# Optimization experiments

Measured on AMD Instinct MI355X. Metric: run time of the kernel, lower is better.

Reference implementation:

```python
import jax, jax.numpy as jnp
import numpy as np

NUM_HEADS = 16
TOP_K = 2
ROPE_BASE = 10000.0
LN_EPS = 1e-5


def _rope_sin_cos(S, D, dtype):
    # D = head_dim; inv_freq over even indices, shape [D//2]
    inv_freq = 1.0 / (ROPE_BASE ** (jnp.arange(0, D, 2, dtype=jnp.float32) / D))
    freqs = jnp.arange(S, dtype=jnp.float32)[:, None] * inv_freq[None, :]  # [S, D//2]
    sin = jnp.sin(freqs).astype(dtype)[None, :, None, :]  # [1,S,1,D//2]
    cos = jnp.cos(freqs).astype(dtype)[None, :, None, :]
    return sin, cos


def _apply_rope(x, sin, cos):
    # x: [B,S,H,D]; rotate interleaved even/odd pairs
    x1, x2 = x[..., 0::2], x[..., 1::2]
    r1 = x1 * cos - x2 * sin
    r2 = x1 * sin + x2 * cos
    return jnp.stack([r1, r2], axis=-1).reshape(x.shape)


def _layer_norm(x, w, b):
    mu = jnp.mean(x, axis=-1, keepdims=True)
    var = jnp.mean(jnp.square(x - mu), axis=-1, keepdims=True)
    return (x - mu) * jax.lax.rsqrt(var + LN_EPS) * w + b


def reference(x, in_proj_w, in_proj_b, out_proj_w, out_proj_b,
              gate_w, gate_b, expert_w, expert_b,
              ln1_w, ln1_b, ln2_w, ln2_b):
    B, S, E = x.shape
    H = NUM_HEADS
    D = E // H

    # --- RoPE on q and k (per-head) ---
    xh = x.reshape(B, S, H, D)
    sin, cos = _rope_sin_cos(S, D, x.dtype)
    q_in = _apply_rope(xh, sin, cos).reshape(B, S, E)
    k_in = q_in  # q = k in the module
    v_in = x

    # --- MultiheadAttention (eval, causal mask) ---
    Wq, Wk, Wv = jnp.split(in_proj_w, 3, axis=0)  # each [E,E]
    bq, bk, bv = jnp.split(in_proj_b, 3, axis=0)
    q = (q_in @ Wq.T + bq).reshape(B, S, H, D)
    k = (k_in @ Wk.T + bk).reshape(B, S, H, D)
    v = (v_in @ Wv.T + bv).reshape(B, S, H, D)

    scale = 1.0 / jnp.sqrt(jnp.asarray(D, dtype=x.dtype))
    scores = jnp.einsum('bqhd,bkhd->bhqk', q, k) * scale  # [B,H,S,S]
    causal = jnp.tril(jnp.ones((S, S), dtype=bool))
    scores = jnp.where(causal[None, None], scores, jnp.asarray(-jnp.inf, dtype=scores.dtype))
    attn = jax.nn.softmax(scores, axis=-1)
    ctx = jnp.einsum('bhqk,bkhd->bqhd', attn, v).reshape(B, S, E)
    attn_out = ctx @ out_proj_w.T + out_proj_b

    x1 = _layer_norm(x + attn_out, ln1_w, ln1_b)

    # --- MoE: dense all-experts compute + top-k gather/combine ---
    gates = jax.nn.softmax(x1 @ gate_w.T + gate_b, axis=-1)  # [B,S,Eexp]
    _, top_idx = jax.lax.top_k(gates, TOP_K)                 # [B,S,K]
    top_gates = jnp.take_along_axis(gates, top_idx, axis=-1)  # differentiable gather
    # expert_outputs: [B,S,Eexp,E]
    expert_outputs = jnp.einsum('bsd,efd->bsef', x1, expert_w) + expert_b[None, None]
    sel = jnp.take_along_axis(
        expert_outputs, top_idx[..., None], axis=2)  # [B,S,K,E]
    moe_out = jnp.sum(sel * top_gates[..., None], axis=2)    # [B,S,E]

    return _layer_norm(x1 + moe_out, ln2_w, ln2_b)


def setup_inputs() -> dict:
    key = jax.random.key(0)
    ks = jax.random.split(key, 8)
    B, S, E, NE = 2, 2048, 1024, 8
    s = 0.02
    return {
        'x': jax.random.normal(ks[0], (B, S, E), dtype=jnp.float32),
        'in_proj_w': jax.random.normal(ks[1], (3 * E, E), dtype=jnp.float32) * s,
        'in_proj_b': jnp.zeros((3 * E,), dtype=jnp.float32),
        'out_proj_w': jax.random.normal(ks[2], (E, E), dtype=jnp.float32) * s,
        'out_proj_b': jnp.zeros((E,), dtype=jnp.float32),
        'gate_w': jax.random.normal(ks[3], (NE, E), dtype=jnp.float32) * s,
        'gate_b': jnp.zeros((NE,), dtype=jnp.float32),
        'expert_w': jax.random.normal(ks[4], (NE, E, E), dtype=jnp.float32) * s,
        'expert_b': jnp.zeros((NE, E), dtype=jnp.float32),
        'ln1_w': jnp.ones((E,), dtype=jnp.float32),
        'ln1_b': jnp.zeros((E,), dtype=jnp.float32),
        'ln2_w': jnp.ones((E,), dtype=jnp.float32),
        'ln2_b': jnp.zeros((E,), dtype=jnp.float32),
    }
```

## Files before the change

### kernel.cpp

```cpp
#include <hip/hip_runtime.h>
#include <hip/hip_bf16.h>
#include <stdint.h>

#define B_  2
#define S_  2048
#define E_  1024
#define H_  16
#define D_  64
#define NE_ 8
#define M_  4096

typedef unsigned short u16;
typedef _Float16 f16x8 __attribute__((ext_vector_type(8)));
typedef float f32x4 __attribute__((ext_vector_type(4)));

__device__ __forceinline__ f32x4 fzero4() { f32x4 v; v[0]=0.f; v[1]=0.f; v[2]=0.f; v[3]=0.f; return v; }

__device__ __forceinline__ u16 hbits(_Float16 h) { union { _Float16 f; u16 u; } c; c.f = h; return c.u; }
__device__ __forceinline__ u16 f2h(float v) { return hbits((_Float16)v); }

__device__ __forceinline__ void storeA3(u16* p, size_t stride, float v) {
  _Float16 h = (_Float16)v; float hf = (float)h;
  p[0]        = hbits(h);
  p[stride]   = f2h(hf * 0.015625f);
  p[2*stride] = f2h((v - hf) * 64.0f);
}
__device__ __forceinline__ void storeW3(u16* p, size_t stride, float v) {
  _Float16 h = (_Float16)v; float hf = (float)h;
  p[0]        = hbits(h);
  p[stride]   = f2h((v - hf) * 64.0f);
  p[2*stride] = f2h(hf * 0.015625f);
}
__device__ __forceinline__ void store2s(u16* p, size_t stride, float v) {
  _Float16 h = (_Float16)v; float hf = (float)h;
  p[0]      = hbits(h);
  p[stride] = f2h((v - hf) * 64.0f);
}

__device__ __forceinline__ void gload_lds16(const void* g, void* l) {
  __builtin_amdgcn_global_load_lds(
      (const __attribute__((address_space(1))) void*)g,
      (__attribute__((address_space(3))) void*)l, 16, 0, 0);
}

#define MFMA16(a, b, c) __builtin_amdgcn_mfma_f32_16x16x32_f16((a), (b), (c), 0, 0, 0)

__global__ __launch_bounds__(256) void k_splitW(const float* __restrict__ in, u16* __restrict__ out, int total) {
  int idx = blockIdx.x * 256 + threadIdx.x;
  if (idx >= total) return;
  int n = idx >> 10, k = idx & 1023;
  storeW3(out + (size_t)n * 3072 + k, 1024, in[idx]);
}

__global__ __launch_bounds__(256) void k_convH(const float* __restrict__ in, u16* __restrict__ out, int total) {
  int idx = blockIdx.x * 256 + threadIdx.x;
  if (idx < total) out[idx] = f2h(in[idx]);
}

__global__ __launch_bounds__(256) void k_rope3(const float* __restrict__ x, u16* __restrict__ ropeA, u16* __restrict__ xA) {
  int p = blockIdx.x * 256 + threadIdx.x;
  if (p >= B_ * S_ * H_ * 32) return;
  int i   = p & 31;
  int h   = (p >> 5) & 15;
  int row = p >> 9;
  int s   = row & (S_ - 1);
  int col = h * 64 + 2 * i;
  size_t base = (size_t)row * E_ + col;
  float x1 = x[base], x2 = x[base + 1];
  float inv = exp2f(-(float)i * 0.41524101186092029f);
  float ang = (float)s * inv;
  float sn, cs; sincosf(ang, &sn, &cs);
  float r1 = x1 * cs - x2 * sn;
  float r2 = x1 * sn + x2 * cs;
  size_t ob = (size_t)row * 3072 + col;
  storeA3(ropeA + ob,     1024, r1);
  storeA3(ropeA + ob + 1, 1024, r2);
  storeA3(xA + ob,        1024, x1);
  storeA3(xA + ob + 1,    1024, x2);
}

__global__ __launch_bounds__(256) void gemm_qkv(
    const u16* __restrict__ ropeA, const u16* __restrict__ xA,
    const u16* __restrict__ Wall, const float* __restrict__ ipb,
    u16* __restrict__ q2, u16* __restrict__ k2, u16* __restrict__ vt2)
{
  __shared__ __align__(16) u16 lA[128 * 32];
  __shared__ __align__(16) u16 lB[128 * 32];
  const int tid  = threadIdx.x;
  const int lane = tid & 63;
  const int wid  = tid >> 6;
  const int nt = blockIdx.x, mt = blockIdx.y;
  const u16* A = (nt < 16) ? ropeA : xA;
  long aoff[2], boff[2];
#pragma unroll
  for (int i = 0; i < 2; ++i) {
    aoff[i] = (long)(mt * 128 + i * 64 + (tid >> 2)) * 3072 + (tid & 3) * 8;
    boff[i] = (long)(nt * 128 + i * 64 + (tid >> 2)) * 3072 + (tid & 3) * 8;
  }
  f32x4 acc[4][4];
#pragma unroll
  for (int a = 0; a < 4; ++a)
#pragma unroll
    for (int b = 0; b < 4; ++b) acc[a][b] = fzero4();
  const int wm = wid >> 1, wn = wid & 1;
  const int r16 = lane & 15, g4 = lane >> 4;

  for (int k0 = 0; k0 < 3072; k0 += 32) {
#pragma unroll
    for (int i = 0; i < 2; ++i) {
      gload_lds16(A    + aoff[i] + k0, (char*)lA + i * 4096 + wid * 1024);
      gload_lds16(Wall + boff[i] + k0, (char*)lB + i * 4096 + wid * 1024);
    }
    __syncthreads();
    f16x8 af[4], bf[4];
#pragma unroll
    for (int f = 0; f < 4; ++f) {
      af[f] = *(const f16x8*)&lA[(wm * 64 + f * 16 + r16) * 32 + 8 * g4];
      bf[f] = *(const f16x8*)&lB[(wn * 64 + f * 16 + r16) * 32 + 8 * g4];
    }
#pragma unroll
    for (int fm = 0; fm < 4; ++fm)
#pragma unroll
      for (int fn = 0; fn < 4; ++fn)
        acc[fm][fn] = MFMA16(af[fm], bf[fn], acc[fm][fn]);
    __syncthreads();
  }

  const int m0 = mt * 128 + wm * 64;
  const int n0 = nt * 128 + wn * 64;
  const size_t PLV = (size_t)B_ * H_ * 64 * S_;
#pragma unroll
  for (int fm = 0; fm < 4; ++fm) {
#pragma unroll
    for (int fn = 0; fn < 4; ++fn) {
      const int colg = n0 + fn * 16 + r16;
      const float bv = ipb[colg];
#pragma unroll
      for (int i = 0; i < 4; ++i) {
        const int rowg = m0 + fm * 16 + 4 * g4 + i;
        float v = acc[fm][fn][i] + bv;
        int bb = rowg >> 11, s = rowg & 2047;
        if (nt < 16) {
          int col = colg & 1023, hh = col >> 6, d = col & 63;
          u16* tgt = (colg < 1024) ? q2 : k2;
          store2s(tgt + (((size_t)(bb * H_ + hh)) * S_ + s) * 128 + d, 64, v);
        } else {
          int col = colg - 2048, hh = col >> 6, d = col & 63;
          store2s(vt2 + (((size_t)(bb * H_ + hh)) * 64 + d) * (size_t)S_ + s, PLV, v);
        }
      }
    }
  }
}

template <int EPI, bool GATHER>
__global__ __launch_bounds__(256) void gemm_bt(
    const u16* __restrict__ A, const u16* __restrict__ Bw,
    const float* __restrict__ bias, void* __restrict__ Cout,
    int M, int N, int K,
    const int* __restrict__ lists, const int* __restrict__ cnt,
    const float* __restrict__ topw)
{
  __shared__ __align__(16) u16 lA[128 * 32];
  __shared__ __align__(16) u16 lB[128 * 32];
  const int tid  = threadIdx.x;
  const int lane = tid & 63;
  const int wid  = tid >> 6;
  const int nt = blockIdx.x, mt = blockIdx.y;
  int cnt_e = 0;
  const int* listE = nullptr;
  if constexpr (GATHER) {
    int e = blockIdx.z;
    cnt_e = cnt[e];
    if (mt * 128 >= cnt_e) return;
    Bw   += (size_t)e * N * K;
    bias += (size_t)e * N;
    listE = lists + e * 4096;
  }
  long aoff[2], boff[2];
#pragma unroll
  for (int i = 0; i < 2; ++i) {
    long arow;
    if constexpr (GATHER) {
      int li = mt * 128 + i * 64 + (tid >> 2);
      int entry = (li < cnt_e) ? listE[li] : 0;
      arow = entry >> 1;
    } else {
      arow = mt * 128 + i * 64 + (tid >> 2);
    }
    aoff[i] = arow * (long)K + (tid & 3) * 8;
    boff[i] = (long)(nt * 128 + i * 64 + (tid >> 2)) * K + (tid & 3) * 8;
  }
  f32x4 acc[4][4];
#pragma unroll
  for (int a = 0; a < 4; ++a)
#pragma unroll
    for (int b = 0; b < 4; ++b) acc[a][b] = fzero4();
  const int wm = wid >> 1, wn = wid & 1;
  const int r16 = lane & 15, g4 = lane >> 4;

  for (int k0 = 0; k0 < K; k0 += 32) {
#pragma unroll
    for (int i = 0; i < 2; ++i) {
      gload_lds16(A  + aoff[i] + k0, (char*)lA + i * 4096 + wid * 1024);
      gload_lds16(Bw + boff[i] + k0, (char*)lB + i * 4096 + wid * 1024);
    }
    __syncthreads();
    f16x8 af[4], bf[4];
#pragma unroll
    for (int f = 0; f < 4; ++f) {
      af[f] = *(const f16x8*)&lA[(wm * 64 + f * 16 + r16) * 32 + 8 * g4];
      bf[f] = *(const f16x8*)&lB[(wn * 64 + f * 16 + r16) * 32 + 8 * g4];
    }
#pragma unroll
    for (int fm = 0; fm < 4; ++fm)
#pragma unroll
      for (int fn = 0; fn < 4; ++fn)
        acc[fm][fn] = MFMA16(af[fm], bf[fn], acc[fm][fn]);
    __syncthreads();
  }

  const int m0 = mt * 128 + wm * 64;
  const int n0 = nt * 128 + wn * 64;
#pragma unroll
  for (int fm = 0; fm < 4; ++fm) {
#pragma unroll
    for (int fn = 0; fn < 4; ++fn) {
      const int colg = n0 + fn * 16 + r16;
      const float bv = bias[colg];
#pragma unroll
      for (int i = 0; i < 4; ++i) {
        const int rowg = m0 + fm * 16 + 4 * g4 + i;
        float v = acc[fm][fn][i] + bv;
        if constexpr (EPI == 2) {
          ((float*)Cout)[(size_t)rowg * N + colg] = v;
        } else {
          if (rowg < cnt_e) {
            int entry = listE[rowg];
            ((float*)Cout)[(size_t)entry * 1024 + colg] = v * topw[entry];
          }
        }
      }
    }
  }
}

__global__ __launch_bounds__(256) void k_attn4(const u16* __restrict__ Q2, const u16* __restrict__ K2,
                                               const u16* __restrict__ VT2, u16* __restrict__ ctx3) {
  __shared__ __align__(16) u16 Kl[2][64 * 128];
  __shared__ __align__(16) u16 Vl[2][2 * 64 * 64];
  __shared__ __align__(16) u16 Pl[4][2 * 1024];
  const int tid  = threadIdx.x;
  const int w    = tid >> 6;
  const int lane = tid & 63;
  const int r16 = lane & 15, g4 = lane >> 4;

  const int bid  = blockIdx.x;
  const int xcd  = bid & 7;
  const int slot = bid >> 3;
  const int bh   = xcd + 8 * (slot >> 5);
  const int qb   = 31 - (slot & 31);
  const int nkt  = qb + 1;

  const size_t PLV = (size_t)B_ * H_ * 64 * S_;
  const u16* Qp = Q2  + (size_t)bh * S_ * 128;
  const u16* Kp = K2  + (size_t)bh * S_ * 128;
  const u16* Vp = VT2 + (size_t)bh * 64 * S_;
  const int qw0 = qb * 64 + w * 16;

  f16x8 qh[2], ql[2];
#pragma unroll
  for (int t = 0; t < 2; ++t) {
    qh[t] = *(const f16x8*)&Qp[(size_t)(qw0 + r16) * 128 + t * 32 + 8 * g4];
    ql[t] = *(const f16x8*)&Qp[(size_t)(qw0 + r16) * 128 + 64 + t * 32 + 8 * g4];
  }

  float mrow[4], lrow[4];
  f32x4 om[4], ox[4];
#pragma unroll
  for (int i = 0; i < 4; ++i) { mrow[i] = -1e30f; lrow[i] = 0.f; }
#pragma unroll
  for (int db = 0; db < 4; ++db) { om[db] = fzero4(); ox[db] = fzero4(); }

  auto STAGE = [&](int buf, int k0) {
#pragma unroll
    for (int c = 0; c < 4; ++c) {
      const int li = c * 4 + w;
      {
        const int row = li * 4 + (lane >> 4);
        const int so  = ((lane & 15) ^ (row & 7)) * 8;
        gload_lds16(Kp + (size_t)(k0 + row) * 128 + so,
                    (char*)&Kl[buf][0] + li * 1024);
      }
      {
        const int plane = li >> 3;
        const int d     = (li & 7) * 8 + (lane >> 3);
        const int so    = ((lane & 7) ^ (d & 7)) * 8;
        gload_lds16(Vp + (size_t)plane * PLV + (size_t)d * S_ + k0 + so,
                    (char*)&Vl[buf][0] + li * 1024);
      }
    }
  };

  STAGE(0, 0);
  __syncthreads();

  for (int kt = 0; kt < nkt; ++kt) {
    const int buf = kt & 1;
    const int k0  = kt * 64;
    if (kt + 1 < nkt) STAGE(buf ^ 1, k0 + 64);

    f32x4 sm[4], sx[4];
#pragma unroll
    for (int ks = 0; ks < 4; ++ks) { sm[ks] = fzero4(); sx[ks] = fzero4(); }
#pragma unroll
    for (int ks = 0; ks < 4; ++ks) {
      const int row = ks * 16 + r16;
#pragma unroll
      for (int t = 0; t < 2; ++t) {
        const int sw = ((t * 4 + g4) ^ (r16 & 7)) * 8;
        f16x8 kh = *(const f16x8*)&Kl[buf][row * 128 + sw];
        f16x8 kl = *(const f16x8*)&Kl[buf][row * 128 + 64 + sw];
        sm[ks] = MFMA16(qh[t], kh, sm[ks]);
        sx[ks] = MFMA16(qh[t], kl, sx[ks]);
        sx[ks] = MFMA16(ql[t], kh, sx[ks]);
      }
    }

    float pv[4][4], corr[4];
#pragma unroll
    for (int i = 0; i < 4; ++i) {
      const int qg = qw0 + 4 * g4 + i;
      float s[4];
      float mx = -1e30f;
#pragma unroll
      for (int ks = 0; ks < 4; ++ks) {
        float v = (sm[ks][i] + sx[ks][i] * 0.015625f) * 0.125f;
        if (k0 + ks * 16 + r16 > qg) v = -1e30f;
        s[ks] = v;
        mx = fmaxf(mx, v);
      }
      mx = fmaxf(mx, __shfl_xor(mx, 1));
      mx = fmaxf(mx, __shfl_xor(mx, 2));
      mx = fmaxf(mx, __shfl_xor(mx, 4));
      mx = fmaxf(mx, __shfl_xor(mx, 8));
      float mn = fmaxf(mrow[i], mx);
      float c  = __expf(mrow[i] - mn);
      float rs = 0.f;
#pragma unroll
      for (int ks = 0; ks < 4; ++ks) {
        float e = __expf(s[ks] - mn);
        pv[ks][i] = e;
        rs += e;
      }
      rs += __shfl_xor(rs, 1);
      rs += __shfl_xor(rs, 2);
      rs += __shfl_xor(rs, 4);
      rs += __shfl_xor(rs, 8);
      lrow[i] = lrow[i] * c + rs;
      mrow[i] = mn;
      corr[i] = c;
    }
#pragma unroll
    for (int db = 0; db < 4; ++db)
#pragma unroll
      for (int i = 0; i < 4; ++i) { om[db][i] *= corr[i]; ox[db][i] *= corr[i]; }

#pragma unroll
    for (int ks = 0; ks < 4; ++ks) {
      const int sl = ks * 2 + (r16 >> 3);
#pragma unroll
      for (int i = 0; i < 4; ++i) {
        const int pr = 4 * g4 + i;
        const int ad = pr * 64 + ((sl ^ (pr & 7)) * 8) + (r16 & 7);
        float p = pv[ks][i];
        _Float16 h = (_Float16)p; float hf = (float)h;
        Pl[w][ad]        = hbits(h);
        Pl[w][1024 + ad] = f2h((p - hf) * 64.0f);
      }
    }
    asm volatile("s_waitcnt lgkmcnt(0)" ::: "memory");
    __builtin_amdgcn_sched_barrier(0);

#pragma unroll
    for (int kk = 0; kk < 2; ++kk) {
      const int psw = ((kk * 4 + g4) ^ (r16 & 7)) * 8;
      f16x8 ph  = *(const f16x8*)&Pl[w][r16 * 64 + psw];
      f16x8 pl2 = *(const f16x8*)&Pl[w][1024 + r16 * 64 + psw];
#pragma unroll
      for (int db = 0; db < 4; ++db) {
        const int d = db * 16 + r16;
        const int vsw = ((kk * 4 + g4) ^ (r16 & 7)) * 8;
        f16x8 vh  = *(const f16x8*)&Vl[buf][d * 64 + vsw];
        f16x8 vl2 = *(const f16x8*)&Vl[buf][4096 + d * 64 + vsw];
        om[db] = MFMA16(ph, vh, om[db]);
        ox[db] = MFMA16(ph, vl2, ox[db]);
        ox[db] = MFMA16(pl2, vh, ox[db]);
      }
    }
    __syncthreads();
  }

  const int b = bh >> 4, h = bh & 15;
#pragma unroll
  for (int db = 0; db < 4; ++db) {
#pragma unroll
    for (int i = 0; i < 4; ++i) {
      const int srow = qw0 + 4 * g4 + i;
      float val = (om[db][i] + ox[db][i] * 0.015625f) / lrow[i];
      size_t rb = ((size_t)(b * S_ + srow)) * 3072 + h * 64 + db * 16 + r16;
      storeA3(ctx3 + rb, 1024, val);
    }
  }
}

__device__ __forceinline__ float block_sum256(float v, float* red) {
#pragma unroll
  for (int off = 32; off > 0; off >>= 1) v += __shfl_down(v, off);
  const int wid = threadIdx.x >> 6;
  if ((threadIdx.x & 63) == 0) red[wid] = v;
  __syncthreads();
  float tot = red[0] + red[1] + red[2] + red[3];
  __syncthreads();
  return tot;
}

__global__ __launch_bounds__(256) void k_ln1(const float* __restrict__ x, const float* __restrict__ ao,
                                             const float* __restrict__ w, const float* __restrict__ bb,
                                             float* __restrict__ x1f, u16* __restrict__ x1h) {
  const int row = blockIdx.x, t = threadIdx.x;
  __shared__ float red[4];
  f32x4 xv = ((const f32x4*)(x  + (size_t)row * 1024))[t];
  f32x4 av = ((const f32x4*)(ao + (size_t)row * 1024))[t];
  f32x4 v  = xv + av;
  float tot = block_sum256(v[0] + v[1] + v[2] + v[3], red);
  float mu = tot * (1.0f / 1024.0f);
  f32x4 d = v - mu;
  float totq = block_sum256(d[0]*d[0] + d[1]*d[1] + d[2]*d[2] + d[3]*d[3], red);
  float rs = rsqrtf(totq * (1.0f / 1024.0f) + 1e-5f);
  f32x4 wv = ((const f32x4*)w)[t];
  f32x4 bv = ((const f32x4*)bb)[t];
  f32x4 o;
#pragma unroll
  for (int j = 0; j < 4; ++j) o[j] = d[j] * rs * wv[j] + bv[j];
  ((f32x4*)(x1f + (size_t)row * 1024))[t] = o;
#pragma unroll
  for (int j = 0; j < 4; ++j) x1h[(size_t)row * 1024 + t * 4 + j] = f2h(o[j]);
}

__global__ __launch_bounds__(256) void k_ln2(const float* __restrict__ x1f, const float* __restrict__ pair,
                                             const float* __restrict__ w, const float* __restrict__ bb,
                                             float* __restrict__ out) {
  const int row = blockIdx.x, t = threadIdx.x;
  __shared__ float red[4];
  f32x4 v  = ((const f32x4*)(x1f + (size_t)row * 1024))[t];
  f32x4 pa = ((const f32x4*)(pair + ((size_t)row * 2)     * 1024))[t];
  f32x4 pb = ((const f32x4*)(pair + ((size_t)row * 2 + 1) * 1024))[t];
  v = v + pa + pb;
  float tot = block_sum256(v[0] + v[1] + v[2] + v[3], red);
  float mu = tot * (1.0f / 1024.0f);
  f32x4 d = v - mu;
  float totq = block_sum256(d[0]*d[0] + d[1]*d[1] + d[2]*d[2] + d[3]*d[3], red);
  float rs = rsqrtf(totq * (1.0f / 1024.0f) + 1e-5f);
  f32x4 wv = ((const f32x4*)w)[t];
  f32x4 bv = ((const f32x4*)bb)[t];
  f32x4 o;
#pragma unroll
  for (int j = 0; j < 4; ++j) o[j] = d[j] * rs * wv[j] + bv[j];
  ((f32x4*)out)[(size_t)row * 256 + t] = o;
}

__global__ __launch_bounds__(64) void k_zero(int* p, int n) {
  int i = threadIdx.x;
  if (i < n) p[i] = 0;
}

__global__ __launch_bounds__(64) void k_gate(const float* __restrict__ x1f,
                                             const float* __restrict__ gw, const float* __restrict__ gb,
                                             float* __restrict__ topw, int* __restrict__ cnt, int* __restrict__ lists) {
  const int t = blockIdx.x, lane = threadIdx.x;
  const f32x4* xr = (const f32x4*)(x1f + (size_t)t * 1024);
  f32x4 xv[4];
#pragma unroll
  for (int c = 0; c < 4; ++c) xv[c] = xr[lane * 4 + c];
  float logit[8];
#pragma unroll
  for (int e = 0; e < 8; ++e) {
    const f32x4* wr = (const f32x4*)(gw + (size_t)e * 1024);
    float a = 0.f;
#pragma unroll
    for (int c = 0; c < 4; ++c) {
      f32x4 wv = wr[lane * 4 + c];
      a += xv[c][0]*wv[0] + xv[c][1]*wv[1] + xv[c][2]*wv[2] + xv[c][3]*wv[3];
    }
#pragma unroll
    for (int off = 32; off > 0; off >>= 1) a += __shfl_xor(a, off);
    logit[e] = a + gb[e];
  }
  if (lane == 0) {
    float mx = logit[0];
#pragma unroll
    for (int e = 1; e < 8; ++e) mx = fmaxf(mx, logit[e]);
    float g[8], se = 0.f;
#pragma unroll
    for (int e = 0; e < 8; ++e) { g[e] = __expf(logit[e] - mx); se += g[e]; }
    float inv = 1.0f / se;
#pragma unroll
    for (int e = 0; e < 8; ++e) g[e] *= inv;
    int e1 = 0;
#pragma unroll
    for (int e = 1; e < 8; ++e) if (g[e] > g[e1]) e1 = e;
    int e2 = (e1 == 0) ? 1 : 0;
#pragma unroll
    for (int e = 0; e < 8; ++e) if (e != e1 && g[e] > g[e2]) e2 = e;
    topw[t * 2]     = g[e1];
    topw[t * 2 + 1] = g[e2];
    int p1 = atomicAdd(&cnt[e1], 1); lists[e1 * 4096 + p1] = t * 2;
    int p2 = atomicAdd(&cnt[e2], 1); lists[e2 * 4096 + p2] = t * 2 + 1;
  }
}

extern "C" void kernel_launch(void* const* d_in, const int* in_sizes, int n_in,
                              void* d_out, int out_size, void* d_ws, size_t ws_size,
                              hipStream_t stream) {
  const float* x    = (const float*)d_in[0];
  const float* ipw  = (const float*)d_in[1];
  const float* ipb  = (const float*)d_in[2];
  const float* opw  = (const float*)d_in[3];
  const float* opb  = (const float*)d_in[4];
  const float* gw   = (const float*)d_in[5];
  const float* gb   = (const float*)d_in[6];
  const float* ew   = (const float*)d_in[7];
  const float* eb   = (const float*)d_in[8];
  const float* ln1w = (const float*)d_in[9];
  const float* ln1b = (const float*)d_in[10];
  const float* ln2w = (const float*)d_in[11];
  const float* ln2b = (const float*)d_in[12];
  char* ws = (char*)d_ws;

  constexpr size_t OF_WQKV = 0;
  constexpr size_t OF_WOUT = OF_WQKV + (size_t)3072*3072*2;
  constexpr size_t OF_WEXP = OF_WOUT + (size_t)1024*3072*2;
  constexpr size_t OF_RA   = OF_WEXP + (size_t)8*1024*1024*2;
  constexpr size_t OF_RB   = OF_RA + (size_t)4096*3072*2;
  constexpr size_t OF_RC   = OF_RB + (size_t)4096*3072*2;
  constexpr size_t OF_RD   = OF_RC + (size_t)16777216;
  constexpr size_t OF_RE   = OF_RD + (size_t)16777216;
  constexpr size_t OF_TOPW = OF_RE + (size_t)16777216;
  constexpr size_t OF_CNT  = OF_TOPW + 32768;
  constexpr size_t OF_LIST = OF_CNT + 256;

  u16*   Wqkv3 = (u16*)(ws + OF_WQKV);
  u16*   Wout3 = (u16*)(ws + OF_WOUT);
  u16*   WexpH = (u16*)(ws + OF_WEXP);
  u16*   rope3 = (u16*)(ws + OF_RA);
  u16*   ctx3  = (u16*)(ws + OF_RA);
  u16*   x3    = (u16*)(ws + OF_RB);
  float* attn  = (float*)(ws + OF_RB);
  u16*   x1h   = (u16*)(ws + OF_RB + (size_t)16777216);
  u16*   q2    = (u16*)(ws + OF_RC);
  float* x1f   = (float*)(ws + OF_RC);
  u16*   k2    = (u16*)(ws + OF_RD);
  u16*   vt2   = (u16*)(ws + OF_RE);
  float* pair  = (float*)(ws + OF_RD);
  float* topw  = (float*)(ws + OF_TOPW);
  int*   cnt   = (int*)(ws + OF_CNT);
  int*   lists = (int*)(ws + OF_LIST);

  (void)in_sizes; (void)n_in; (void)out_size; (void)ws_size;

  k_splitW<<<dim3((3072*1024)/256), 256, 0, stream>>>(ipw, Wqkv3, 3072*1024);
  k_splitW<<<dim3((1024*1024)/256), 256, 0, stream>>>(opw, Wout3, 1024*1024);
  k_convH <<<dim3((8*1024*1024)/256), 256, 0, stream>>>(ew, WexpH, 8*1024*1024);
  k_rope3 <<<dim3(2097152/256), 256, 0, stream>>>(x, rope3, x3);

  gemm_qkv<<<dim3(24, 32), 256, 0, stream>>>(rope3, x3, Wqkv3, ipb, q2, k2, vt2);

  k_attn4<<<dim3(1024), 256, 0, stream>>>(q2, k2, vt2, ctx3);

  gemm_bt<2,false><<<dim3(8,32), 256, 0, stream>>>(ctx3, Wout3, opb, attn, M_, 1024, 3072, nullptr, nullptr, nullptr);

  k_ln1<<<dim3(M_), 256, 0, stream>>>(x, attn, ln1w, ln1b, x1f, x1h);

  k_zero<<<1, 64, 0, stream>>>(cnt, 8);
  k_gate<<<dim3(M_), 64, 0, stream>>>(x1f, gw, gb, topw, cnt, lists);

  gemm_bt<3,true><<<dim3(8,32,8), 256, 0, stream>>>(x1h, WexpH, eb, pair, M_, 1024, 1024, lists, cnt, topw);

  k_ln2<<<dim3(M_), 256, 0, stream>>>(x1f, pair, ln2w, ln2b, (float*)d_out);
}
```

Baseline: 664.6 us.

## Halve GEMM N-tile to 64 and rebalance causal attention block ordering

The GEMM kernel gains a BN template parameter, and the out-projection and expert GEMMs now use 64-wide N tiles with twice as many blocks. This gives more waves on the 256-CU device, which suits grids that were small (256 blocks) or sparse because of gathering, at the cost of less B-tile reuse per block. Attention block scheduling now alternates query-block order by round and rotates it on later rounds. The aim is to balance causal work across XCDs and time instead of always launching heavy blocks first.

```diff
diff --git a/kernel.cpp b/kernel.cpp
--- a/kernel.cpp
+++ b/kernel.cpp
@@ -153,7 +153,7 @@
   }
 }
 
-template <int EPI, bool GATHER>
+template <int EPI, bool GATHER, int BN>
 __global__ __launch_bounds__(256) void gemm_bt(
     const u16* __restrict__ A, const u16* __restrict__ Bw,
     const float* __restrict__ bias, void* __restrict__ Cout,
@@ -161,8 +161,10 @@
     const int* __restrict__ lists, const int* __restrict__ cnt,
     const float* __restrict__ topw)
 {
+  constexpr int BCH = BN / 64;
+  constexpr int FN  = BN / 32;
   __shared__ __align__(16) u16 lA[128 * 32];
-  __shared__ __align__(16) u16 lB[128 * 32];
+  __shared__ __align__(16) u16 lB[BN * 32];
   const int tid  = threadIdx.x;
   const int lane = tid & 63;
   const int wid  = tid >> 6;
@@ -177,7 +179,7 @@
     bias += (size_t)e * N;
     listE = lists + e * 4096;
   }
-  long aoff[2], boff[2];
+  long aoff[2], boff[BCH];
 #pragma unroll
   for (int i = 0; i < 2; ++i) {
     long arow;
@@ -189,43 +191,48 @@
       arow = mt * 128 + i * 64 + (tid >> 2);
     }
     aoff[i] = arow * (long)K + (tid & 3) * 8;
-    boff[i] = (long)(nt * 128 + i * 64 + (tid >> 2)) * K + (tid & 3) * 8;
-  }
-  f32x4 acc[4][4];
+  }
+#pragma unroll
+  for (int i = 0; i < BCH; ++i)
+    boff[i] = (long)(nt * BN + i * 64 + (tid >> 2)) * K + (tid & 3) * 8;
+
+  f32x4 acc[4][FN];
 #pragma unroll
   for (int a = 0; a < 4; ++a)
 #pragma unroll
-    for (int b = 0; b < 4; ++b) acc[a][b] = fzero4();
+    for (int b = 0; b < FN; ++b) acc[a][b] = fzero4();
   const int wm = wid >> 1, wn = wid & 1;
   const int r16 = lane & 15, g4 = lane >> 4;
 
   for (int k0 = 0; k0 < K; k0 += 32) {
 #pragma unroll
-    for (int i = 0; i < 2; ++i) {
-      gload_lds16(A  + aoff[i] + k0, (char*)lA + i * 4096 + wid * 1024);
+    for (int i = 0; i < 2; ++i)
+      gload_lds16(A + aoff[i] + k0, (char*)lA + i * 4096 + wid * 1024);
+#pragma unroll
+    for (int i = 0; i < BCH; ++i)
       gload_lds16(Bw + boff[i] + k0, (char*)lB + i * 4096 + wid * 1024);
-    }
     __syncthreads();
-    f16x8 af[4], bf[4];
-#pragma unroll
-    for (int f = 0; f < 4; ++f) {
+    f16x8 af[4], bf[FN];
+#pragma unroll
+    for (int f = 0; f < 4; ++f)
       af[f] = *(const f16x8*)&lA[(wm * 64 + f * 16 + r16) * 32 + 8 * g4];
-      bf[f] = *(const f16x8*)&lB[(wn * 64 + f * 16 + r16) * 32 + 8 * g4];
-    }
+#pragma unroll
+    for (int f = 0; f < FN; ++f)
+      bf[f] = *(const f16x8*)&lB[(wn * (FN * 16) + f * 16 + r16) * 32 + 8 * g4];
 #pragma unroll
     for (int fm = 0; fm < 4; ++fm)
 #pragma unroll
-      for (int fn = 0; fn < 4; ++fn)
+      for (int fn = 0; fn < FN; ++fn)
         acc[fm][fn] = MFMA16(af[fm], bf[fn], acc[fm][fn]);
     __syncthreads();
   }
 
   const int m0 = mt * 128 + wm * 64;
-  const int n0 = nt * 128 + wn * 64;
+  const int n0 = nt * BN + wn * (FN * 16);
 #pragma unroll
   for (int fm = 0; fm < 4; ++fm) {
 #pragma unroll
-    for (int fn = 0; fn < 4; ++fn) {
+    for (int fn = 0; fn < FN; ++fn) {
       const int colg = n0 + fn * 16 + r16;
       const float bv = bias[colg];
 #pragma unroll
@@ -258,8 +265,11 @@
   const int bid  = blockIdx.x;
   const int xcd  = bid & 7;
   const int slot = bid >> 3;
-  const int bh   = xcd + 8 * (slot >> 5);
-  const int qb   = 31 - (slot & 31);
+  const int rnd  = slot >> 5;
+  const int c    = slot & 31;
+  const int bh   = xcd + 8 * rnd;
+  const int cc   = (rnd >= 2) ? ((c + 8) & 31) : c;
+  const int qb   = (rnd & 1) ? cc : (31 - cc);
   const int nkt  = qb + 1;
 
   const size_t PLV = (size_t)B_ * H_ * 64 * S_;
@@ -284,8 +294,8 @@
 
   auto STAGE = [&](int buf, int k0) {
 #pragma unroll
-    for (int c = 0; c < 4; ++c) {
-      const int li = c * 4 + w;
+    for (int c4 = 0; c4 < 4; ++c4) {
+      const int li = c4 * 4 + w;
       {
         const int row = li * 4 + (lane >> 4);
         const int so  = ((lane & 15) ^ (row & 7)) * 8;
@@ -345,7 +355,7 @@
       mx = fmaxf(mx, __shfl_xor(mx, 4));
       mx = fmaxf(mx, __shfl_xor(mx, 8));
       float mn = fmaxf(mrow[i], mx);
-      float c  = __expf(mrow[i] - mn);
+      float cr = __expf(mrow[i] - mn);
       float rs = 0.f;
 #pragma unroll
       for (int ks = 0; ks < 4; ++ks) {
@@ -357,9 +367,9 @@
       rs += __shfl_xor(rs, 2);
       rs += __shfl_xor(rs, 4);
       rs += __shfl_xor(rs, 8);
-      lrow[i] = lrow[i] * c + rs;
+      lrow[i] = lrow[i] * cr + rs;
       mrow[i] = mn;
-      corr[i] = c;
+      corr[i] = cr;
     }
 #pragma unroll
     for (int db = 0; db < 4; ++db)
@@ -578,14 +588,14 @@
 
   k_attn4<<<dim3(1024), 256, 0, stream>>>(q2, k2, vt2, ctx3);
 
-  gemm_bt<2,false><<<dim3(8,32), 256, 0, stream>>>(ctx3, Wout3, opb, attn, M_, 1024, 3072, nullptr, nullptr, nullptr);
+  gemm_bt<2,false,64><<<dim3(16,32), 256, 0, stream>>>(ctx3, Wout3, opb, attn, M_, 1024, 3072, nullptr, nullptr, nullptr);
 
   k_ln1<<<dim3(M_), 256, 0, stream>>>(x, attn, ln1w, ln1b, x1f, x1h);
 
   k_zero<<<1, 64, 0, stream>>>(cnt, 8);
   k_gate<<<dim3(M_), 64, 0, stream>>>(x1f, gw, gb, topw, cnt, lists);
 
-  gemm_bt<3,true><<<dim3(8,32,8), 256, 0, stream>>>(x1h, WexpH, eb, pair, M_, 1024, 1024, lists, cnt, topw);
+  gemm_bt<3,true,64><<<dim3(16,32,8), 256, 0, stream>>>(x1h, WexpH, eb, pair, M_, 1024, 1024, lists, cnt, topw);
 
   k_ln2<<<dim3(M_), 256, 0, stream>>>(x1f, pair, ln2w, ln2b, (float*)d_out);
 }
```

Measured after the change: 651.6 us. Within noise of the previous version (-1.9%).
